# Performance work log

Measured on AMD Instinct MI355X. Metric: run time of the kernel, lower is better.

## Reference

```python
import jax, jax.numpy as jnp
import numpy as np
from jax import lax

SIGMA = 0.2
SPACING = 3
EPS = 1e-8

def multinomial_pool(prob, key, spacing=SPACING):
    """Stochastic multinomial max-pool over spacing x spacing blocks.
    Returns (sparse_detection [B,C,H,W], pooled_map [B,C,H/s,W/s], winner [B,C,H/s,W/s] int)."""
    B, C, H, W = prob.shape
    s = spacing
    Hb, Wb = H // s, W // s
    # [B,C,Hb,Wb,s*s]
    blocks = prob.reshape(B, C, Hb, s, Wb, s).transpose(0, 1, 2, 4, 3, 5).reshape(B, C, Hb, Wb, s * s)
    logits = jnp.log(blocks + EPS)
    g = jax.random.gumbel(key, blocks.shape, dtype=prob.dtype)
    winner = jnp.argmax(logits + g, axis=-1)                      # [B,C,Hb,Wb]
    onehot = jax.nn.one_hot(winner, s * s, dtype=prob.dtype)      # [B,C,Hb,Wb,s*s]
    sparse_blocks = blocks * onehot
    pooled = jnp.sum(sparse_blocks, axis=-1)                      # prob at winner
    sparse = sparse_blocks.reshape(B, C, Hb, Wb, s, s).transpose(0, 1, 2, 4, 3, 5).reshape(B, C, H, W)
    return sparse, pooled, winner

def crbm_layer(x, W, b, key):
    pre = lax.conv_general_dilated(x, W, window_strides=(1, 1), padding='VALID',
                                   dimension_numbers=('NCHW', 'OIHW', 'NCHW'))
    pre = (pre + b[None, :, None, None]) / (SIGMA ** 2)
    prob = jax.nn.sigmoid(pre)
    _, pooled, _ = multinomial_pool(prob, key)
    return pooled

def setup_inputs() -> dict:
    key = jax.random.key(0)
    kx, k1, k2 = jax.random.split(key, 3)
    x = jax.random.uniform(kx, (64, 3, 96, 96), dtype=jnp.float32)
    W1 = jax.random.normal(k1, (96, 3, 7, 7), dtype=jnp.float32) * 0.1
    b1 = jnp.zeros((96,), dtype=jnp.float32)
    W2 = jax.random.normal(k2, (192, 96, 7, 7), dtype=jnp.float32) * 0.1
    b2 = jnp.zeros((192,), dtype=jnp.float32)
    return {"x": x, "W1": W1, "b1": b1, "W2": W2, "b2": b2}

def reference(x, W1, b1, W2, b2):
    key = jax.random.key(42)
    kp1, kp2 = jax.random.split(key)
    h1 = crbm_layer(x, W1, b1, kp1)    # [64,96,30,30]
    h2 = crbm_layer(h1, W2, b2, kp2)   # [64,192,8,8]
    return h2
```

## Files before the change

kernel.cpp:

```cpp
#include <hip/hip_runtime.h>
#include <cstdint>
#include <math.h>


#define EPS_D 1e-8
#define INV_SIGMA2 (1.0 / (0.2 * 0.2))
#define TAU 6e-3
#define TAU1 2e-3f
#define RTH1 0.9980020f
#define RTH2 0.9940180f
#define REDO_CAP 32768
#define H1_BYTES (5529600ull * 8ull)
#define H1F32_BYTES (5529600ull * 4ull)
#define HB16_PLANE 5529600ull
#define HB16_BYTES (2ull * HB16_PLANE * 2ull)
#define WSPLIT_ELEMS (49ull * 192ull * 96ull)
#define XSPL_PLANE 2359296ull
#define XSPL_BYTES (3ull * XSPL_PLANE * 2ull)
#define W1B_BYTES (7ull * 3ull * 96ull * 32ull * 2ull)
#define RUNION_BYTES (XSPL_BYTES + W1B_BYTES)

typedef __bf16 bf16x8 __attribute__((ext_vector_type(8)));
typedef __bf16 bf16x4 __attribute__((ext_vector_type(4)));
typedef float f32x4 __attribute__((ext_vector_type(4)));

#define MFMA(A_, B_, C_) \
  __builtin_amdgcn_mfma_f32_16x16x32_bf16((A_), (B_), (C_), 0, 0, 0)

__host__ __device__ __forceinline__ void threefry2x32(
    uint32_t k0, uint32_t k1, uint32_t x0, uint32_t x1,
    uint32_t* o0, uint32_t* o1) {
  const uint32_t ks0 = k0, ks1 = k1, ks2 = k0 ^ k1 ^ 0x1BD11BDAu;
  x0 += ks0; x1 += ks1;
#define TF_R(r) { x0 += x1; x1 = (x1 << (r)) | (x1 >> (32 - (r))); x1 ^= x0; }
  TF_R(13) TF_R(15) TF_R(26) TF_R(6)
  x0 += ks1; x1 += ks2 + 1u;
  TF_R(17) TF_R(29) TF_R(16) TF_R(24)
  x0 += ks2; x1 += ks0 + 2u;
  TF_R(13) TF_R(15) TF_R(26) TF_R(6)
  x0 += ks0; x1 += ks1 + 3u;
  TF_R(17) TF_R(29) TF_R(16) TF_R(24)
  x0 += ks1; x1 += ks2 + 4u;
  TF_R(13) TF_R(15) TF_R(26) TF_R(6)
  x0 += ks2; x1 += ks0 + 5u;
#undef TF_R
  *o0 = x0; *o1 = x1;
}

__device__ __forceinline__ double fast_log(double x) {
  long long ib = __double_as_longlong(x);
  int e = (int)((ib >> 52) & 0x7ff) - 1023;
  double r = __longlong_as_double((ib & 0xfffffffffffffLL) | 0x3ff0000000000000LL);
  if (r > 1.4142135623730951) { r *= 0.5; e += 1; }
  double s = (r - 1.0) / (r + 1.0);
  double s2 = s * s;
  double t = fma(s2, fma(s2, fma(s2, fma(s2, fma(s2, fma(s2,
      1.0/15.0, 1.0/13.0), 1.0/11.0), 1.0/9.0), 1.0/7.0), 1.0/5.0), 1.0/3.0);
  double lr = fma(2.0 * s * s2, t, 2.0 * s);
  return fma((double)e, 0.6931471805599453, lr);
}

__device__ __forceinline__ double fast_exp(double x) {
  double nd = rint(x * 1.4426950408889634);
  double f = fma(nd, -0.6931471803691238, x);
  f = fma(nd, -1.9082149292705877e-10, f);
  double p = 2.505210838544172e-8;
  p = fma(p, f, 2.755731922398589e-7);
  p = fma(p, f, 2.7557319223985893e-6);
  p = fma(p, f, 2.48015873015873e-5);
  p = fma(p, f, 1.984126984126984e-4);
  p = fma(p, f, 1.3888888888888889e-3);
  p = fma(p, f, 8.333333333333333e-3);
  p = fma(p, f, 4.1666666666666664e-2);
  p = fma(p, f, 0.16666666666666666);
  p = fma(p, f, 0.5);
  p = fma(p, f, 1.0);
  p = fma(p, f, 1.0);
  return ldexp(p, (int)nd);
}

__device__ __forceinline__ double gumbel_pool9(const double (&acc)[9],
                                               double bb, uint64_t base,
                                               uint32_t kp0, uint32_t kp1) {
  double bestv = -1e308, bA = 1.0, bQ = 0.0;
#pragma unroll
  for (int k = 0; k < 9; ++k) {
    double pre = (acc[k] + bb) * INV_SIGMA2;
    double q = fast_exp(-fabs(pre));
    double A = pre >= 0.0 ? 1.0 : q;
    double opq = 1.0 + q;
    double L = fast_log(fma(EPS_D, opq, A)) - fast_log(opq);
    uint32_t o0, o1;
    uint64_t idx = base + (uint64_t)k;
    threefry2x32(kp0, kp1, (uint32_t)(idx >> 32), (uint32_t)idx, &o0, &o1);
    uint32_t bits = o0 ^ o1;
    float u = __uint_as_float((bits >> 9) | 0x3f800000u) - 1.0f;
    if (u == 0.0f) u = 1.17549435e-38f;
    float lg1 = (float)fast_log((double)u);
    double lg2 = fast_log(-(double)lg1);
    float gf = -(float)lg2;
    double v = L + (double)gf;
    if (v > bestv) { bestv = v; bA = A; bQ = q; }
  }
  return bA / (1.0 + bQ);
}

__device__ __forceinline__ float gumbel_pool9_ratio(
    const float (&acc)[9], float bb, uint32_t base,
    uint32_t kp0, uint32_t kp1, bool* flag, float rthresh) {
  float bestr = -1.0f, second = -1.0f, bA = 1.0f, bQ = 0.0f;
#pragma unroll
  for (int k = 0; k < 9; ++k) {
    float pre = (acc[k] + bb) * 25.0f;
    float q = __expf(-fabsf(pre));
    float A = pre >= 0.0f ? 1.0f : q;
    float opq = 1.0f + q;
    float num = fmaf(1e-8f, opq, A);
    uint32_t o0, o1;
    threefry2x32(kp0, kp1, 0u, base + (uint32_t)k, &o0, &o1);
    uint32_t bits = o0 ^ o1;
    float u = __uint_as_float((bits >> 9) | 0x3f800000u) - 1.0f;
    if (u == 0.0f) u = 1.17549435e-38f;
    float m = -__logf(u);
    float r = num / (opq * m);
    if (r > bestr) { second = bestr; bestr = r; bA = A; bQ = q; }
    else if (r > second) second = r;
  }
  *flag = !(second <= bestr * rthresh);
  return bA / (1.0f + bQ);
}

__device__ __forceinline__ unsigned short f32_to_bf16(float v) {
  uint32_t u = __float_as_uint(v);
  return (unsigned short)((u + 0x7fffu + ((u >> 16) & 1u)) >> 16);
}
__device__ __forceinline__ float bf16_to_f32(unsigned short s) {
  return __uint_as_float(((uint32_t)s) << 16);
}

template <int LDSTRIDE, typename T>
__device__ __forceinline__ void conv_pair(const T* __restrict__ xb,
                                          const double (&w)[49],
                                          double (&a0)[9], double (&a1)[9]) {
#pragma unroll
  for (int pr = 0; pr < 12; ++pr) {
    double xr[9];
#pragma unroll
    for (int c = 0; c < 9; ++c) xr[c] = (double)xb[pr * LDSTRIDE + c];
#pragma unroll
    for (int ki = 0; ki < 3; ++ki) {
      const int u0 = pr - ki;
      if (u0 >= 0 && u0 <= 6) {
#pragma unroll
        for (int kj = 0; kj < 3; ++kj)
#pragma unroll
          for (int v = 0; v < 7; ++v)
            a0[ki * 3 + kj] = fma(xr[kj + v], w[u0 * 7 + v], a0[ki * 3 + kj]);
      }
      const int u1 = pr - 3 - ki;
      if (u1 >= 0 && u1 <= 6) {
#pragma unroll
        for (int kj = 0; kj < 3; ++kj)
#pragma unroll
          for (int v = 0; v < 7; ++v)
            a1[ki * 3 + kj] = fma(xr[kj + v], w[u1 * 7 + v], a1[ki * 3 + kj]);
      }
    }
  }
}

__global__ void init_cnt_kernel(unsigned int* __restrict__ cnt) {
  cnt[0] = 0u; cnt[1] = 0u;
}

__global__ __launch_bounds__(256, 3) void l1_kernel(
    const float* __restrict__ x, const float* __restrict__ W1,
    const float* __restrict__ b1, double* __restrict__ h1,
    float* __restrict__ h1f32, int write_f64, int write_f32,
    unsigned int* __restrict__ cnt, uint32_t kp0, uint32_t kp1) {
  const int oc   = blockIdx.x;
  const int b    = blockIdx.y;
  const int half = blockIdx.z;
  const int t = threadIdx.x;
  const int wave = t >> 6;

  if (cnt && oc == 0 && b == 0 && half == 0 && t == 0) *cnt = 0u;

  __shared__ float xs[54 * 96];

  const int p0 = 14 * half;
  const bool active = t < 240;
  const int q = t / 30, bw = t - q * 30;
  const float* xb = xs + (6 * q) * 96 + 3 * bw;

  double a0[9] = {}, a1[9] = {};
  double w[49];

#pragma unroll 1
  for (int ic = 0; ic < 3; ++ic) {
    __syncthreads();
    {
      const char* gsrc = (const char*)(x + ((size_t)b * 3 + ic) * 9216 + (3 * p0) * 96);
#pragma unroll
      for (int p = 0; p < 6; ++p) {
        int elt = p * 256 + t;
        if (elt < 1296) {
          __builtin_amdgcn_global_load_lds(
              (const __attribute__((address_space(1))) void*)(gsrc + (size_t)elt * 16),
              (__attribute__((address_space(3))) void*)((char*)xs +
                                                        (size_t)(p * 256 + wave * 64) * 16),
              16, 0, 0);
        }
      }
    }
    __syncthreads();
    {
      const float* __restrict__ wsrc = W1 + (oc * 3 + ic) * 49;
#pragma unroll
      for (int j = 0; j < 49; ++j) w[j] = (double)wsrc[j];
    }
    if (active) conv_pair<96, float>(xb, w, a0, a1);
  }

  if (active) {
    const double bb = (double)b1[oc];
    const int bh0 = p0 + 2 * q;
#pragma unroll
    for (int j = 0; j < 2; ++j) {
      const int pos = (bh0 + j) * 30 + bw;
      const uint64_t base = ((uint64_t)((b * 96 + oc) * 900 + pos)) * 9ull;
      double pooled = gumbel_pool9(j ? a1 : a0, bb, base, kp0, kp1);
      const size_t oidx = (size_t)(b * 96 + oc) * 900 + pos;
      if (write_f64) h1[oidx] = pooled;
      if (write_f32) h1f32[oidx] = (float)pooled;
    }
  }
}

__global__ __launch_bounds__(256) void x_split_kernel(
    const float* __restrict__ x, unsigned short* __restrict__ xs) {
  int idx = blockIdx.x * 256 + threadIdx.x;
  int px = idx % 96; int rest = idx / 96;
  int row = rest % 96; int b = rest / 96;
  unsigned long long pk[3] = {0ull, 0ull, 0ull};
#pragma unroll
  for (int ic = 0; ic < 3; ++ic) {
    float v = x[((size_t)(b * 3 + ic) * 96 + row) * 96 + px];
    unsigned short s0 = f32_to_bf16(v); float r1 = v - bf16_to_f32(s0);
    unsigned short s1 = f32_to_bf16(r1); float r2 = r1 - bf16_to_f32(s1);
    unsigned short s2 = f32_to_bf16(r2);
    pk[0] |= (unsigned long long)s0 << (16 * ic);
    pk[1] |= (unsigned long long)s1 << (16 * ic);
    pk[2] |= (unsigned long long)s2 << (16 * ic);
  }
#pragma unroll
  for (int p = 0; p < 3; ++p)
    *(unsigned long long*)(xs + (size_t)p * XSPL_PLANE + (size_t)idx * 4) = pk[p];
}

__global__ __launch_bounds__(256) void w1_split_kernel(
    const float* __restrict__ W1, unsigned short* __restrict__ wb) {
  int idx = blockIdx.x * 256 + threadIdx.x;
  int k = idx % 32; int rest = idx / 32;
  int oc = rest % 96; int kh = rest / 96;
  int kw = k >> 2, ic = k & 3;
  float v = (ic < 3 && kw < 7) ? W1[(((size_t)oc * 3 + ic) * 7 + kh) * 7 + kw] : 0.0f;
  unsigned short a = f32_to_bf16(v); float r1 = v - bf16_to_f32(a);
  unsigned short b = f32_to_bf16(r1); float r2 = r1 - bf16_to_f32(b);
  unsigned short c = f32_to_bf16(r2);
  wb[((size_t)(kh * 3 + 0) * 96 + oc) * 32 + k] = a;
  wb[((size_t)(kh * 3 + 1) * 96 + oc) * 32 + k] = b;
  wb[((size_t)(kh * 3 + 2) * 96 + oc) * 32 + k] = c;
}

__global__ __launch_bounds__(256) void w2_split_kernel(
    const float* __restrict__ W2, unsigned short* __restrict__ s0,
    unsigned short* __restrict__ s1, unsigned short* __restrict__ s2) {
  int idx = blockIdx.x * 256 + threadIdx.x;
  int ic = idx % 96; int rest = idx / 96;
  int oc = rest % 192; int tap = rest / 192;
  float v = W2[(size_t)(oc * 96 + ic) * 49 + tap];
  unsigned short a = f32_to_bf16(v); float r1 = v - bf16_to_f32(a);
  unsigned short b = f32_to_bf16(r1); float r2 = r1 - bf16_to_f32(b);
  unsigned short c = f32_to_bf16(r2);
  s0[idx] = a; s1[idx] = b; s2[idx] = c;
}

__global__ __launch_bounds__(256, 2) void l1_mfma_kernel(
    const unsigned short* __restrict__ xs, const unsigned short* __restrict__ wb,
    const float* __restrict__ b1, float* __restrict__ h1f32,
    unsigned short* __restrict__ hb16,
    unsigned int* __restrict__ cnt, unsigned int* __restrict__ list,
    uint32_t kp0, uint32_t kp1) {
  const int xt = blockIdx.x;
  const int yt = blockIdx.y;
  const int b  = blockIdx.z;
  const int t = threadIdx.x;
  const int w = t >> 6;
  const int l = t & 63;
  const int g = l >> 4;
  const int lr = l & 15;
  const int x0 = 30 * xt;
  const int y0 = 6 * yt;

  __shared__ __align__(16) float smem_f[17640];
  char* smem = (char*)smem_f;

  if (t < 4) smem_f[2592 + t] = 0.0f;

  {
    const int wave64 = w << 6;
#pragma unroll
    for (int p = 0; p < 3; ++p) {
      int s = p * 256 + t;
      if (s < 648) {
        int pl = s / 216;
        int r2 = s - pl * 216;
        int row = r2 / 18;
        int ch = r2 - row * 18;
        const char* src = (const char*)(xs + (size_t)pl * XSPL_PLANE +
                          ((size_t)((b * 96 + y0 + row) * 96 + x0)) * 4) + ch * 16;
        __builtin_amdgcn_global_load_lds(
            (const __attribute__((address_space(1))) void*)src,
            (__attribute__((address_space(3))) void*)(smem + (size_t)(p * 256 + wave64) * 16),
            16, 0, 0);
      }
    }
  }

  int aoff[3];
#pragma unroll
  for (int mf = 0; mf < 3; ++mf) {
    int pos = (w * 3 + mf) * 16 + lr;
    if (pos > 179) pos = 179;
    int ya = pos / 30, xxa = pos - 30 * ya;
    aoff[mf] = ya * 288 + xxa * 8 + g * 16;
  }

  f32x4 acc[3][6];
#pragma unroll
  for (int mf = 0; mf < 3; ++mf)
#pragma unroll
    for (int nf = 0; nf < 6; ++nf) acc[mf][nf] = (f32x4){0.f, 0.f, 0.f, 0.f};

  __syncthreads();

#pragma unroll 1
  for (int kh = 0; kh < 7; ++kh) {
    bf16x8 bc[6][3];
#pragma unroll
    for (int nf = 0; nf < 6; ++nf) {
      int oc = nf * 16 + lr;
#pragma unroll
      for (int pl = 0; pl < 3; ++pl)
        bc[nf][pl] = *(const bf16x8*)&wb[(((size_t)kh * 3 + pl) * 96 + oc) * 32 + 8 * g];
    }
#pragma unroll
    for (int mf = 0; mf < 3; ++mf) {
      const char* ap = smem + kh * 288 + aoff[mf];
      bf16x4 a0l = *(const bf16x4*)(ap);
      bf16x4 a0h = *(const bf16x4*)(ap + 8);
      bf16x4 a1l = *(const bf16x4*)(ap + 3456);
      bf16x4 a1h = *(const bf16x4*)(ap + 3464);
      bf16x4 a2l = *(const bf16x4*)(ap + 6912);
      bf16x4 a2h = *(const bf16x4*)(ap + 6920);
      bf16x8 a0 = __builtin_shufflevector(a0l, a0h, 0, 1, 2, 3, 4, 5, 6, 7);
      bf16x8 a1 = __builtin_shufflevector(a1l, a1h, 0, 1, 2, 3, 4, 5, 6, 7);
      bf16x8 a2 = __builtin_shufflevector(a2l, a2h, 0, 1, 2, 3, 4, 5, 6, 7);
#pragma unroll
      for (int nf = 0; nf < 6; ++nf) {
        f32x4 c = acc[mf][nf];
        c = MFMA(a0, bc[nf][0], c);
        c = MFMA(a0, bc[nf][1], c);
        c = MFMA(a1, bc[nf][0], c);
        c = MFMA(a1, bc[nf][1], c);
        c = MFMA(a0, bc[nf][2], c);
        c = MFMA(a2, bc[nf][0], c);
        acc[mf][nf] = c;
      }
    }
  }

  __syncthreads();
  {
#pragma unroll
    for (int mf = 0; mf < 3; ++mf)
#pragma unroll
      for (int nf = 0; nf < 6; ++nf)
#pragma unroll
        for (int r = 0; r < 4; ++r) {
          int pos = (w * 3 + mf) * 16 + g * 4 + r;
          if (pos < 180) smem_f[pos * 98 + nf * 16 + lr] = acc[mf][nf][r];
        }
  }
  __syncthreads();

#pragma unroll 1
  for (int i = 0; i < 8; ++i) {
    int oi = i * 256 + t;
    if (oi < 1920) {
      int oc = oi % 96; int rc = oi / 96;
      int pc = rc % 10, pr = rc / 10;
      float a[9];
      float chk = 0.0f;
#pragma unroll
      for (int dy = 0; dy < 3; ++dy)
#pragma unroll
        for (int dx = 0; dx < 3; ++dx) {
          float v = smem_f[((pr * 3 + dy) * 30 + pc * 3 + dx) * 98 + oc];
          a[dy * 3 + dx] = v;
          chk += v;
        }
      int gy = yt * 2 + pr, gx = xt * 10 + pc;
      int pos = gy * 30 + gx;
      unsigned int oidx = (unsigned int)((b * 96 + oc) * 900 + pos);
      bool flag;
      float pooled = gumbel_pool9_ratio(a, b1[oc], oidx * 9u,
                                        kp0, kp1, &flag, RTH1);
      h1f32[oidx] = pooled;
      unsigned short s0 = f32_to_bf16(pooled);
      float r1 = pooled - bf16_to_f32(s0);
      unsigned short s1 = f32_to_bf16(r1);
      size_t nidx = ((size_t)b * 900 + pos) * 96 + oc;
      hb16[nidx] = s0;
      hb16[HB16_PLANE + nidx] = s1;
      if (flag || chk != chk) {
        unsigned int idx = atomicAdd(cnt, 1u);
        if (idx < REDO_CAP) list[idx] = oidx;
      }
    }
  }
}

__global__ __launch_bounds__(64) void l1_redo_kernel(
    const float* __restrict__ x, const float* __restrict__ W1,
    const float* __restrict__ b1, float* __restrict__ h1f32,
    unsigned short* __restrict__ hb16,
    const unsigned int* __restrict__ cnt, const unsigned int* __restrict__ list,
    uint32_t kp0, uint32_t kp1) {
  unsigned int n = *cnt;
  if (n > REDO_CAP) n = REDO_CAP;
  if (blockIdx.x >= n) return;
  const unsigned int oidx = list[blockIdx.x];
  const int gx = oidx % 30;
  const int gy = (oidx / 30) % 30;
  const int rest = oidx / 900;
  const int oc = rest % 96, b = rest / 96;
  const int lane = threadIdx.x;

  double acc[9] = {};
  if (lane < 49) {
    const int kh = lane / 7, kw = lane % 7;
#pragma unroll
    for (int ic = 0; ic < 3; ++ic) {
      double wv = (double)W1[(((size_t)oc * 3 + ic) * 7 + kh) * 7 + kw];
      const float* __restrict__ xp = x + ((size_t)(b * 3 + ic) * 96) * 96;
#pragma unroll
      for (int dy = 0; dy < 3; ++dy)
#pragma unroll
        for (int dx = 0; dx < 3; ++dx) {
          int y = 3 * gy + dy + kh, xc = 3 * gx + dx + kw;
          acc[dy * 3 + dx] = fma((double)xp[(size_t)y * 96 + xc], wv, acc[dy * 3 + dx]);
        }
    }
  }
#pragma unroll
  for (int off = 32; off; off >>= 1)
#pragma unroll
    for (int k = 0; k < 9; ++k) acc[k] += __shfl_down(acc[k], off);

  if (lane == 0) {
    double pooled = gumbel_pool9(acc, (double)b1[oc], (uint64_t)oidx * 9ull,
                                 kp0, kp1);
    float pf = (float)pooled;
    h1f32[oidx] = pf;
    unsigned short s0 = f32_to_bf16(pf);
    float r1 = pf - bf16_to_f32(s0);
    unsigned short s1 = f32_to_bf16(r1);
    size_t nidx = ((size_t)b * 900 + gy * 30 + gx) * 96 + oc;
    hb16[nidx] = s0;
    hb16[HB16_PLANE + nidx] = s1;
  }
}

__global__ __launch_bounds__(256, 3) void l2_mfma_kernel(
    const unsigned short* __restrict__ hb16,
    const unsigned short* __restrict__ wp0,
    const unsigned short* __restrict__ wp1,
    const unsigned short* __restrict__ wp2, float* __restrict__ conv,
    int b_base) {
  const int nt = blockIdx.x;
  const int my = blockIdx.y;
  const int b_local = my / 3, mt = my - 3 * b_local;
  const int b = b_base + b_local;
  const int t = threadIdx.x;
  const int l = t & 63;
  const int w = t >> 6;
  const int wm = w >> 1, wn = w & 1;
  const int g = l >> 4;
  const int lr = l & 15;
  const int wave64 = w << 6;

  __shared__ __align__(16) unsigned short As2[2 * 4 * 420 * 8];

  int rowoff[6];
#pragma unroll
  for (int mf = 0; mf < 6; ++mf) {
    int ml = wm * 96 + mf * 16 + lr;
    int yl = ml / 24, xx = ml - 24 * yl;
    rowoff[mf] = g * 6720 + (yl * 30 + xx) * 16;
  }
  const int oc0 = nt * 64 + wn * 32 + lr;

  f32x4 acc[6][2];
#pragma unroll
  for (int mf = 0; mf < 6; ++mf)
#pragma unroll
    for (int nf = 0; nf < 2; ++nf) acc[mf][nf] = (f32x4){0.f, 0.f, 0.f, 0.f};

  const size_t pixbase = ((size_t)b * 900 + 240 * (size_t)mt) * 96;

#pragma unroll 1
  for (int ch = 0; ch < 3; ++ch) {
    __syncthreads();
#pragma unroll
    for (int i = 0; i < 14; ++i) {
      int s = i * 256 + t;
      if (s < 3360) {
        int pl = s / 1680;
        int r = s - pl * 1680;
        int g2 = r / 420;
        int px = r - g2 * 420;
        const unsigned short* src = hb16 + (size_t)pl * HB16_PLANE + pixbase +
                                    (size_t)px * 96 + ch * 32 + g2 * 8;
        __builtin_amdgcn_global_load_lds(
            (const __attribute__((address_space(1))) void*)src,
            (__attribute__((address_space(3))) void*)((char*)As2 +
                                                      (size_t)(i * 256 + wave64) * 16),
            16, 0, 0);
      }
    }
    __syncthreads();

    int boff = oc0 * 96 + ch * 32 + 8 * g;
    bf16x8 bc[2][3], bn[2][3];
#pragma unroll
    for (int nf = 0; nf < 2; ++nf) {
      bc[nf][0] = *(const bf16x8*)&wp0[boff + nf * 1536];
      bc[nf][1] = *(const bf16x8*)&wp1[boff + nf * 1536];
      bc[nf][2] = *(const bf16x8*)&wp2[boff + nf * 1536];
    }
    int kh = 0, kw = 0;
#pragma unroll 1
    for (int tap = 0; tap < 49; ++tap) {
      if (tap < 48) {
        const int bo2 = boff + 18432;
#pragma unroll
        for (int nf = 0; nf < 2; ++nf) {
          bn[nf][0] = *(const bf16x8*)&wp0[bo2 + nf * 1536];
          bn[nf][1] = *(const bf16x8*)&wp1[bo2 + nf * 1536];
          bn[nf][2] = *(const bf16x8*)&wp2[bo2 + nf * 1536];
        }
        boff = bo2;
      }
      const int tapoff = (kh * 30 + kw) * 16;
#pragma unroll
      for (int mf = 0; mf < 6; ++mf) {
        const char* ap = (const char*)As2 + rowoff[mf] + tapoff;
        bf16x8 a0 = *(const bf16x8*)(ap);
        bf16x8 a1 = *(const bf16x8*)(ap + 26880);
#pragma unroll
        for (int nf = 0; nf < 2; ++nf) {
          f32x4 c = acc[mf][nf];
          c = MFMA(a0, bc[nf][0], c);
          c = MFMA(a0, bc[nf][1], c);
          c = MFMA(a1, bc[nf][0], c);
          c = MFMA(a1, bc[nf][1], c);
          c = MFMA(a0, bc[nf][2], c);
          acc[mf][nf] = c;
        }
      }
      if (tap < 48) {
#pragma unroll
        for (int nf = 0; nf < 2; ++nf)
#pragma unroll
          for (int s = 0; s < 3; ++s) bc[nf][s] = bn[nf][s];
      }
      if (++kw == 7) { kw = 0; ++kh; }
    }
  }

  const int rowsub = g * 4;
#pragma unroll
  for (int mf = 0; mf < 6; ++mf)
#pragma unroll
    for (int nf = 0; nf < 2; ++nf)
#pragma unroll
      for (int r = 0; r < 4; ++r) {
        const int m_abs = mt * 192 + wm * 96 + mf * 16 + rowsub + r;
        const int oc = oc0 + nf * 16;
        conv[((size_t)b_local * 576 + m_abs) * 192 + oc] = acc[mf][nf][r];
      }
}

__global__ __launch_bounds__(192) void l2_pool_kernel(
    const float* __restrict__ conv, const float* __restrict__ b2,
    float* __restrict__ out, unsigned int* __restrict__ cnt,
    unsigned int* __restrict__ list, uint32_t kp0, uint32_t kp1, int b_base) {
  const int pos = blockIdx.x;
  const int bl = blockIdx.y;
  const int b = b_base + bl;
  const int oc = threadIdx.x;
  const int ph = pos >> 3, pw = pos & 7;
  float a[9];
  float chk = 0.0f;
  const float* __restrict__ cb = conv + (size_t)bl * 576 * 192 + oc;
#pragma unroll
  for (int dy = 0; dy < 3; ++dy)
#pragma unroll
    for (int dx = 0; dx < 3; ++dx) {
      float v = cb[((size_t)((3 * ph + dy) * 24 + 3 * pw + dx)) * 192];
      a[dy * 3 + dx] = v;
      chk += v;
    }
  const unsigned int oid = (unsigned int)((b * 192 + oc) * 64 + pos);
  bool flag;
  float pooled = gumbel_pool9_ratio(a, b2[oc], oid * 9u, kp0, kp1, &flag, RTH2);
  out[oid] = pooled;
  if (flag || chk != chk) {
    unsigned int idx = atomicAdd(cnt, 1u);
    if (idx < REDO_CAP) list[idx] = oid;
  }
}

__global__ __launch_bounds__(256, 3) void l2_kernel_f64(
    const double* __restrict__ h1, const float* __restrict__ W2,
    const float* __restrict__ b2, float* __restrict__ out,
    uint32_t kp0, uint32_t kp1) {
  const int octile = blockIdx.x;
  const int b      = blockIdx.y;
  const int t = threadIdx.x;
  const int wave = t >> 6;
  const int oc_local = t >> 5;
  const int li = t & 31;
  const int bw = li & 7;
  const int ph = 2 * ((li >> 3) & 1) + (li >> 4);
  const int bh0 = 2 * ph;
  const int oc = octile * 8 + oc_local;

  __shared__ double hs[2][900];
  __shared__ double wsd[2][392];

  const double* __restrict__ hb = h1 + (size_t)b * 86400;
  const float* __restrict__ wg = W2 + (size_t)octile * 8 * 4704;

  double a0[9] = {}, a1[9] = {};
  double w[49];

  auto stage = [&](int c, int buf) {
    const char* gsrc = (const char*)(hb + (size_t)c * 900);
#pragma unroll
    for (int p = 0; p < 2; ++p) {
      int elt = p * 256 + t;
      if (elt < 450) {
        __builtin_amdgcn_global_load_lds(
            (const __attribute__((address_space(1))) void*)(gsrc + (size_t)elt * 16),
            (__attribute__((address_space(3))) void*)((char*)&hs[buf][0] +
                                                      (size_t)(p * 256 + wave * 64) * 16),
            16, 0, 0);
      }
    }
#pragma unroll
    for (int p = 0; p < 2; ++p) {
      int j = p * 256 + t;
      if (j < 392) {
        int oi = j / 49, rem = j - oi * 49;
        wsd[buf][j] = (double)wg[(size_t)oi * 4704 + c * 49 + rem];
      }
    }
  };

  stage(0, 0);
#pragma unroll 1
  for (int c = 0; c < 96; ++c) {
    __syncthreads();
    if (c + 1 < 96) stage(c + 1, (c + 1) & 1);
    {
      const double* __restrict__ wsrc = &wsd[c & 1][oc_local * 49];
#pragma unroll
      for (int j = 0; j < 49; ++j) w[j] = wsrc[j];
      const double* xb = &hs[c & 1][(6 * ph) * 30 + 3 * bw];
      conv_pair<30, double>(xb, w, a0, a1);
    }
  }

  const double bb = (double)b2[oc];
#pragma unroll
  for (int j = 0; j < 2; ++j) {
    const int bh = bh0 + j;
    const uint64_t base = ((uint64_t)(((b * 192 + oc) * 8 + bh) * 8 + bw)) * 9ull;
    double pooled = gumbel_pool9(j ? a1 : a0, bb, base, kp0, kp1);
    out[(size_t)(b * 192 + oc) * 64 + bh * 8 + bw] = (float)pooled;
  }
}

__global__ __launch_bounds__(64) void l2_redo_kernel(
    const float* __restrict__ h1f, const float* __restrict__ W2,
    const float* __restrict__ b2, float* __restrict__ out,
    const unsigned int* __restrict__ cnt, const unsigned int* __restrict__ list,
    uint32_t kp0, uint32_t kp1) {
  unsigned int n = *cnt;
  if (n > REDO_CAP) n = REDO_CAP;
  if (blockIdx.x >= n) return;
  const unsigned int oid = list[blockIdx.x];
  const int sp = oid & 63, bh = sp >> 3, bw = sp & 7;
  const int rest = oid >> 6, oc = rest % 192, b = rest / 192;
  const int lane = threadIdx.x;

  double acc[9] = {};
  for (int ic = lane; ic < 96; ic += 64) {
    const float* __restrict__ xp =
        h1f + ((size_t)(b * 96 + ic) * 30 + 3 * bh) * 30 + 3 * bw;
    const float* __restrict__ wp = W2 + ((size_t)oc * 96 + ic) * 49;
    double w[49];
#pragma unroll
    for (int j = 0; j < 49; ++j) w[j] = (double)wp[j];
#pragma unroll
    for (int pr = 0; pr < 9; ++pr) {
      double xr[9];
#pragma unroll
      for (int c = 0; c < 9; ++c) xr[c] = (double)xp[pr * 30 + c];
#pragma unroll
      for (int kh = 0; kh < 3; ++kh) {
        const int u = pr - kh;
        if (u >= 0 && u <= 6) {
#pragma unroll
          for (int kw = 0; kw < 3; ++kw)
#pragma unroll
            for (int v = 0; v < 7; ++v)
              acc[kh * 3 + kw] = fma(xr[kw + v], w[u * 7 + v], acc[kh * 3 + kw]);
        }
      }
    }
  }
#pragma unroll
  for (int off = 32; off; off >>= 1)
#pragma unroll
    for (int k = 0; k < 9; ++k) acc[k] += __shfl_down(acc[k], off);

  if (lane == 0) {
    const uint64_t base = (uint64_t)oid * 9ull;
    double pooled = gumbel_pool9(acc, (double)b2[oc], base, kp0, kp1);
    out[oid] = (float)pooled;
  }
}

extern "C" void kernel_launch(void* const* d_in, const int* in_sizes, int n_in,
                              void* d_out, int out_size, void* d_ws,
                              size_t ws_size, hipStream_t stream) {
  const float* x  = (const float*)d_in[0];
  const float* W1 = (const float*)d_in[1];
  const float* b1 = (const float*)d_in[2];
  const float* W2 = (const float*)d_in[3];
  const float* b2 = (const float*)d_in[4];
  float* out = (float*)d_out;

  uint32_t kp1a, kp1b, kp2a, kp2b;
  threefry2x32(0u, 42u, 0u, 0u, &kp1a, &kp1b);
  threefry2x32(0u, 42u, 0u, 1u, &kp2a, &kp2b);

  const size_t WSPL_BYTES = WSPLIT_ELEMS * 2ull;
  const size_t need_main = H1F32_BYTES + HB16_BYTES + RUNION_BYTES +
                           3 * WSPL_BYTES + 16 + 2 * (size_t)REDO_CAP * 4;
  const size_t need_f64  = H1_BYTES;

  if (ws_size >= need_main) {
    char* wsb = (char*)d_ws;
    float* h1f32 = (float*)wsb;
    unsigned short* hb16 = (unsigned short*)(wsb + H1F32_BYTES);
    char* R = wsb + H1F32_BYTES + HB16_BYTES;
    unsigned short* xsplit = (unsigned short*)R;
    unsigned short* w1b = (unsigned short*)(R + XSPL_BYTES);
    float* conv = (float*)R;
    unsigned short* wp0 = (unsigned short*)(R + RUNION_BYTES);
    unsigned short* wp1 = wp0 + WSPLIT_ELEMS;
    unsigned short* wp2 = wp1 + WSPLIT_ELEMS;
    unsigned int* cntblk = (unsigned int*)(R + RUNION_BYTES + 3 * WSPL_BYTES);
    unsigned int* list1 = cntblk + 4;
    unsigned int* list2 = list1 + REDO_CAP;

    init_cnt_kernel<<<1, 1, 0, stream>>>(cntblk);
    x_split_kernel<<<2304, 256, 0, stream>>>(x, xsplit);
    w1_split_kernel<<<84, 256, 0, stream>>>(W1, w1b);
    w2_split_kernel<<<3528, 256, 0, stream>>>(W2, wp0, wp1, wp2);
    l1_mfma_kernel<<<dim3(3, 15, 64), 256, 0, stream>>>(
        xsplit, w1b, b1, h1f32, hb16, cntblk + 0, list1, kp1a, kp1b);
    l1_redo_kernel<<<REDO_CAP, 64, 0, stream>>>(
        x, W1, b1, h1f32, hb16, cntblk + 0, list1, kp1a, kp1b);
    l2_mfma_kernel<<<dim3(3, 96), 256, 0, stream>>>(hb16, wp0, wp1, wp2,
                                                    conv, 0);
    l2_pool_kernel<<<dim3(64, 32), 192, 0, stream>>>(conv, b2, out,
                                                     cntblk + 1, list2,
                                                     kp2a, kp2b, 0);
    l2_mfma_kernel<<<dim3(3, 96), 256, 0, stream>>>(hb16, wp0, wp1, wp2,
                                                    conv, 32);
    l2_pool_kernel<<<dim3(64, 32), 192, 0, stream>>>(conv, b2, out,
                                                     cntblk + 1, list2,
                                                     kp2a, kp2b, 32);
    l2_redo_kernel<<<REDO_CAP, 64, 0, stream>>>(h1f32, W2, b2, out,
                                                cntblk + 1, list2, kp2a, kp2b);
  } else {
    double* h1 = (double*)d_ws;
    l1_kernel<<<dim3(96, 64, 2), 256, 0, stream>>>(
        x, W1, b1, h1, (float*)0, 1, 0, (unsigned int*)0, kp1a, kp1b);
    l2_kernel_f64<<<dim3(24, 64), 256, 0, stream>>>(h1, W2, b2, out,
                                                    kp2a, kp2b);
  }
}
```

Measured before the change: 874.5 us.

## Drop fp32 h1 copy, store third bf16 plane, merge layer-2 halves

Layer 1 no longer writes a separate fp32 h1 array. It stores a third bf16 residual plane, and the layer-2 redo kernel rebuilds h1 from the three bf16 planes. The freed workspace lets the layer-2 MFMA and pool kernels run once over the full batch instead of in two halves, when enough workspace is available. The layer-2 grid axes are also swapped so adjacent blocks share the same batch tile. The aim is to cut launches and fp32 write traffic, at the cost of an extra bf16 plane write and a larger conv buffer.

```diff
diff --git a/kernel.cpp b/kernel.cpp
--- a/kernel.cpp
+++ b/kernel.cpp
@@ -11,14 +11,15 @@
 #define RTH2 0.9940180f
 #define REDO_CAP 32768
 #define H1_BYTES (5529600ull * 8ull)
-#define H1F32_BYTES (5529600ull * 4ull)
 #define HB16_PLANE 5529600ull
-#define HB16_BYTES (2ull * HB16_PLANE * 2ull)
+#define HB3_BYTES (3ull * HB16_PLANE * 2ull)
+#define CONV_FULL (64ull * 576ull * 192ull * 4ull)
+#define CONV_HALF (32ull * 576ull * 192ull * 4ull)
 #define WSPLIT_ELEMS (49ull * 192ull * 96ull)
 #define XSPL_PLANE 2359296ull
 #define XSPL_BYTES (3ull * XSPL_PLANE * 2ull)
 #define W1B_BYTES (7ull * 3ull * 96ull * 32ull * 2ull)
-#define RUNION_BYTES (XSPL_BYTES + W1B_BYTES)
+#define RUNION_HALF (XSPL_BYTES + W1B_BYTES)
 
 typedef __bf16 bf16x8 __attribute__((ext_vector_type(8)));
 typedef __bf16 bf16x4 __attribute__((ext_vector_type(4)));
@@ -176,15 +177,12 @@
 __global__ __launch_bounds__(256, 3) void l1_kernel(
     const float* __restrict__ x, const float* __restrict__ W1,
     const float* __restrict__ b1, double* __restrict__ h1,
-    float* __restrict__ h1f32, int write_f64, int write_f32,
-    unsigned int* __restrict__ cnt, uint32_t kp0, uint32_t kp1) {
+    uint32_t kp0, uint32_t kp1) {
   const int oc   = blockIdx.x;
   const int b    = blockIdx.y;
   const int half = blockIdx.z;
   const int t = threadIdx.x;
   const int wave = t >> 6;
-
-  if (cnt && oc == 0 && b == 0 && half == 0 && t == 0) *cnt = 0u;
 
   __shared__ float xs[54 * 96];
 
@@ -231,8 +229,7 @@
       const uint64_t base = ((uint64_t)((b * 96 + oc) * 900 + pos)) * 9ull;
       double pooled = gumbel_pool9(j ? a1 : a0, bb, base, kp0, kp1);
       const size_t oidx = (size_t)(b * 96 + oc) * 900 + pos;
-      if (write_f64) h1[oidx] = pooled;
-      if (write_f32) h1f32[oidx] = (float)pooled;
+      h1[oidx] = pooled;
     }
   }
 }
@@ -288,8 +285,7 @@
 
 __global__ __launch_bounds__(256, 2) void l1_mfma_kernel(
     const unsigned short* __restrict__ xs, const unsigned short* __restrict__ wb,
-    const float* __restrict__ b1, float* __restrict__ h1f32,
-    unsigned short* __restrict__ hb16,
+    const float* __restrict__ b1, unsigned short* __restrict__ hb16,
     unsigned int* __restrict__ cnt, unsigned int* __restrict__ list,
     uint32_t kp0, uint32_t kp1) {
   const int xt = blockIdx.x;
@@ -417,13 +413,15 @@
       bool flag;
       float pooled = gumbel_pool9_ratio(a, b1[oc], oidx * 9u,
                                         kp0, kp1, &flag, RTH1);
-      h1f32[oidx] = pooled;
       unsigned short s0 = f32_to_bf16(pooled);
       float r1 = pooled - bf16_to_f32(s0);
       unsigned short s1 = f32_to_bf16(r1);
+      float r2 = r1 - bf16_to_f32(s1);
+      unsigned short s2 = f32_to_bf16(r2);
       size_t nidx = ((size_t)b * 900 + pos) * 96 + oc;
       hb16[nidx] = s0;
       hb16[HB16_PLANE + nidx] = s1;
+      hb16[2 * HB16_PLANE + nidx] = s2;
       if (flag || chk != chk) {
         unsigned int idx = atomicAdd(cnt, 1u);
         if (idx < REDO_CAP) list[idx] = oidx;
@@ -434,8 +432,7 @@
 
 __global__ __launch_bounds__(64) void l1_redo_kernel(
     const float* __restrict__ x, const float* __restrict__ W1,
-    const float* __restrict__ b1, float* __restrict__ h1f32,
-    unsigned short* __restrict__ hb16,
+    const float* __restrict__ b1, unsigned short* __restrict__ hb16,
     const unsigned int* __restrict__ cnt, const unsigned int* __restrict__ list,
     uint32_t kp0, uint32_t kp1) {
   unsigned int n = *cnt;
@@ -473,13 +470,15 @@
     double pooled = gumbel_pool9(acc, (double)b1[oc], (uint64_t)oidx * 9ull,
                                  kp0, kp1);
     float pf = (float)pooled;
-    h1f32[oidx] = pf;
     unsigned short s0 = f32_to_bf16(pf);
     float r1 = pf - bf16_to_f32(s0);
     unsigned short s1 = f32_to_bf16(r1);
+    float r2 = r1 - bf16_to_f32(s1);
+    unsigned short s2 = f32_to_bf16(r2);
     size_t nidx = ((size_t)b * 900 + gy * 30 + gx) * 96 + oc;
     hb16[nidx] = s0;
     hb16[HB16_PLANE + nidx] = s1;
+    hb16[2 * HB16_PLANE + nidx] = s2;
   }
 }
 
@@ -489,8 +488,8 @@
     const unsigned short* __restrict__ wp1,
     const unsigned short* __restrict__ wp2, float* __restrict__ conv,
     int b_base) {
-  const int nt = blockIdx.x;
-  const int my = blockIdx.y;
+  const int my = blockIdx.x;
+  const int nt = blockIdx.y;
   const int b_local = my / 3, mt = my - 3 * b_local;
   const int b = b_base + b_local;
   const int t = threadIdx.x;
@@ -705,7 +704,7 @@
 }
 
 __global__ __launch_bounds__(64) void l2_redo_kernel(
-    const float* __restrict__ h1f, const float* __restrict__ W2,
+    const unsigned short* __restrict__ hb16, const float* __restrict__ W2,
     const float* __restrict__ b2, float* __restrict__ out,
     const unsigned int* __restrict__ cnt, const unsigned int* __restrict__ list,
     uint32_t kp0, uint32_t kp1) {
@@ -719,8 +718,6 @@
 
   double acc[9] = {};
   for (int ic = lane; ic < 96; ic += 64) {
-    const float* __restrict__ xp =
-        h1f + ((size_t)(b * 96 + ic) * 30 + 3 * bh) * 30 + 3 * bw;
     const float* __restrict__ wp = W2 + ((size_t)oc * 96 + ic) * 49;
     double w[49];
 #pragma unroll
@@ -729,7 +726,13 @@
     for (int pr = 0; pr < 9; ++pr) {
       double xr[9];
 #pragma unroll
-      for (int c = 0; c < 9; ++c) xr[c] = (double)xp[pr * 30 + c];
+      for (int c = 0; c < 9; ++c) {
+        size_t idx = ((size_t)b * 900 +
+                      (size_t)((3 * bh + pr) * 30 + 3 * bw + c)) * 96 + ic;
+        float h = (bf16_to_f32(hb16[idx]) + bf16_to_f32(hb16[HB16_PLANE + idx]))
+                  + bf16_to_f32(hb16[2 * HB16_PLANE + idx]);
+        xr[c] = (double)h;
+      }
 #pragma unroll
       for (int kh = 0; kh < 3; ++kh) {
         const int u = pr - kh;
@@ -770,22 +773,24 @@
   threefry2x32(0u, 42u, 0u, 1u, &kp2a, &kp2b);
 
   const size_t WSPL_BYTES = WSPLIT_ELEMS * 2ull;
-  const size_t need_main = H1F32_BYTES + HB16_BYTES + RUNION_BYTES +
-                           3 * WSPL_BYTES + 16 + 2 * (size_t)REDO_CAP * 4;
-  const size_t need_f64  = H1_BYTES;
-
-  if (ws_size >= need_main) {
+  const size_t LISTS = 16 + 2ull * REDO_CAP * 4;
+  const size_t need_merged = HB3_BYTES + CONV_FULL + 3 * WSPL_BYTES + LISTS;
+  const size_t need_half = HB3_BYTES + RUNION_HALF + 3 * WSPL_BYTES + LISTS;
+  const size_t need_f64 = H1_BYTES;
+
+  if (ws_size >= need_half) {
+    const bool merged = ws_size >= need_merged;
     char* wsb = (char*)d_ws;
-    float* h1f32 = (float*)wsb;
-    unsigned short* hb16 = (unsigned short*)(wsb + H1F32_BYTES);
-    char* R = wsb + H1F32_BYTES + HB16_BYTES;
+    unsigned short* hb16 = (unsigned short*)wsb;
+    char* R = wsb + HB3_BYTES;
     unsigned short* xsplit = (unsigned short*)R;
     unsigned short* w1b = (unsigned short*)(R + XSPL_BYTES);
     float* conv = (float*)R;
-    unsigned short* wp0 = (unsigned short*)(R + RUNION_BYTES);
+    const size_t rsz = merged ? CONV_FULL : RUNION_HALF;
+    unsigned short* wp0 = (unsigned short*)(R + rsz);
     unsigned short* wp1 = wp0 + WSPLIT_ELEMS;
     unsigned short* wp2 = wp1 + WSPLIT_ELEMS;
-    unsigned int* cntblk = (unsigned int*)(R + RUNION_BYTES + 3 * WSPL_BYTES);
+    unsigned int* cntblk = (unsigned int*)(R + rsz + 3 * WSPL_BYTES);
     unsigned int* list1 = cntblk + 4;
     unsigned int* list2 = list1 + REDO_CAP;
 
@@ -794,25 +799,32 @@
     w1_split_kernel<<<84, 256, 0, stream>>>(W1, w1b);
     w2_split_kernel<<<3528, 256, 0, stream>>>(W2, wp0, wp1, wp2);
     l1_mfma_kernel<<<dim3(3, 15, 64), 256, 0, stream>>>(
-        xsplit, w1b, b1, h1f32, hb16, cntblk + 0, list1, kp1a, kp1b);
+        xsplit, w1b, b1, hb16, cntblk + 0, list1, kp1a, kp1b);
     l1_redo_kernel<<<REDO_CAP, 64, 0, stream>>>(
-        x, W1, b1, h1f32, hb16, cntblk + 0, list1, kp1a, kp1b);
-    l2_mfma_kernel<<<dim3(3, 96), 256, 0, stream>>>(hb16, wp0, wp1, wp2,
-                                                    conv, 0);
-    l2_pool_kernel<<<dim3(64, 32), 192, 0, stream>>>(conv, b2, out,
-                                                     cntblk + 1, list2,
-                                                     kp2a, kp2b, 0);
-    l2_mfma_kernel<<<dim3(3, 96), 256, 0, stream>>>(hb16, wp0, wp1, wp2,
-                                                    conv, 32);
-    l2_pool_kernel<<<dim3(64, 32), 192, 0, stream>>>(conv, b2, out,
-                                                     cntblk + 1, list2,
-                                                     kp2a, kp2b, 32);
-    l2_redo_kernel<<<REDO_CAP, 64, 0, stream>>>(h1f32, W2, b2, out,
+        x, W1, b1, hb16, cntblk + 0, list1, kp1a, kp1b);
+    if (merged) {
+      l2_mfma_kernel<<<dim3(192, 3), 256, 0, stream>>>(hb16, wp0, wp1, wp2,
+                                                       conv, 0);
+      l2_pool_kernel<<<dim3(64, 64), 192, 0, stream>>>(conv, b2, out,
+                                                       cntblk + 1, list2,
+                                                       kp2a, kp2b, 0);
+    } else {
+      l2_mfma_kernel<<<dim3(96, 3), 256, 0, stream>>>(hb16, wp0, wp1, wp2,
+                                                      conv, 0);
+      l2_pool_kernel<<<dim3(64, 32), 192, 0, stream>>>(conv, b2, out,
+                                                       cntblk + 1, list2,
+                                                       kp2a, kp2b, 0);
+      l2_mfma_kernel<<<dim3(96, 3), 256, 0, stream>>>(hb16, wp0, wp1, wp2,
+                                                      conv, 32);
+      l2_pool_kernel<<<dim3(64, 32), 192, 0, stream>>>(conv, b2, out,
+                                                       cntblk + 1, list2,
+                                                       kp2a, kp2b, 32);
+    }
+    l2_redo_kernel<<<REDO_CAP, 64, 0, stream>>>(hb16, W2, b2, out,
                                                 cntblk + 1, list2, kp2a, kp2b);
-  } else {
+  } else if (ws_size >= need_f64) {
     double* h1 = (double*)d_ws;
-    l1_kernel<<<dim3(96, 64, 2), 256, 0, stream>>>(
-        x, W1, b1, h1, (float*)0, 1, 0, (unsigned int*)0, kp1a, kp1b);
+    l1_kernel<<<dim3(96, 64, 2), 256, 0, stream>>>(x, W1, b1, h1, kp1a, kp1b);
     l2_kernel_f64<<<dim3(24, 64), 256, 0, stream>>>(h1, W2, b2, out,
                                                     kp2a, kp2b);
   }
```

Measured after the change: 861.5 us. Within noise of the previous version (-1.5%).
